# Optimization experiments

Measured on AMD Instinct MI355X. Metric: run time of the kernel, lower is better.

## Reference

```python
import jax, jax.numpy as jnp
import numpy as np

N_NODES = 100000
N_EDGES = 1600000
F_IN = 128
F_OUT = 32
HEADS = 8
ALPHA = 0.2  # LeakyReLU slope


def setup_inputs() -> dict:
    key = jax.random.key(0)
    ks = jax.random.split(key, 7)
    x = jax.random.normal(ks[0], (N_NODES, F_IN), dtype=jnp.float32)
    row = jnp.sort(jax.random.randint(ks[1], (N_EDGES,), 0, N_NODES, dtype=jnp.int32))
    col = jax.random.randint(ks[2], (N_EDGES,), 0, N_NODES, dtype=jnp.int32)
    kernels = jax.random.normal(ks[3], (HEADS, F_IN, F_OUT), dtype=jnp.float32) * 0.1
    att_self = jax.random.normal(ks[4], (HEADS, F_OUT), dtype=jnp.float32) * 0.1
    att_neigh = jax.random.normal(ks[5], (HEADS, F_OUT), dtype=jnp.float32) * 0.1
    biases = jax.random.normal(ks[6], (HEADS, F_OUT), dtype=jnp.float32) * 0.1
    return {"x": x, "row": row, "col": col, "kernels": kernels,
            "att_self": att_self, "att_neigh": att_neigh, "biases": biases}


def reference(x, row, col, kernels, att_self, att_neigh, biases):
    # GraphAttention (GAT), eval mode (dropout inactive), concat over heads.
    N = x.shape[0]
    outs = []
    for h in range(kernels.shape[0]):  # fixed small head loop
        feat = x @ kernels[h]                     # [N, F_OUT]
        a_s = feat @ att_self[h]                  # [N]
        a_n = feat @ att_neigh[h]                 # [N]
        e = a_s[row] + a_n[col]                   # [E] edge logits (SDDMM)
        e = jnp.where(e > 0, e, ALPHA * e)        # LeakyReLU(0.2)
        # row-wise (destination-node) sparse softmax, numerically stable
        m = jax.ops.segment_max(e, row, num_segments=N)
        ex = jnp.exp(e - m[row])
        denom = jax.ops.segment_sum(ex, row, num_segments=N)
        alpha = ex / denom[row]                   # [E]
        # SpMM: out[i] = sum_{e: row[e]=i} alpha[e] * feat[col[e]]
        msg = alpha[:, None] * feat[col]          # [E, F_OUT]
        out = jax.ops.segment_sum(msg, row, num_segments=N) + biases[h]
        outs.append(out)
    return jnp.concatenate(outs, axis=1)          # [N, HEADS*F_OUT]
```

## Files before the change

kernel.cpp:

```cpp
#include <hip/hip_runtime.h>
#include <hip/hip_bf16.h>
#include <math.h>


#define F_IN   128
#define F_ALL  256
#define HEADS  8
#define F_OUT  32
#define ALPHA  0.2f

using f32x4  = __attribute__((ext_vector_type(4))) float;
using bf16x8 = __attribute__((ext_vector_type(8))) short;

static __device__ __forceinline__ unsigned short f32_to_bf16(float f) {
  union { float f; unsigned u; } v; v.f = f;
  unsigned r = v.u + 0x7FFF + ((v.u >> 16) & 1);
  return (unsigned short)(r >> 16);
}
static __device__ __forceinline__ unsigned cvt_pk_bf16(float lo, float hi) {
  unsigned r;
  asm("v_cvt_pk_bf16_f32 %0, %1, %2" : "=v"(r) : "v"(lo), "v"(hi));
  return r;
}
static __device__ __forceinline__ float bf16_lo(unsigned d) {
  return __uint_as_float(d << 16);
}
static __device__ __forceinline__ float bf16_hi(unsigned d) {
  return __uint_as_float(d & 0xffff0000u);
}

__global__ __launch_bounds__(256) void prep0(const float* __restrict__ kern,
                                             const float* __restrict__ att_s,
                                             const float* __restrict__ att_n,
                                             const int* __restrict__ row,
                                             unsigned short* __restrict__ Wt,
                                             float* __restrict__ ws,
                                             float* __restrict__ wn,
                                             int* __restrict__ ptr,
                                             int N, int E) {
  int id = blockIdx.x * 256 + threadIdx.x;
  if (id < 2 * HEADS * F_IN) {
    int which = id >> 10;
    int hk = id & 1023;
    int h = hk >> 7, k = hk & 127;
    const float* att = which ? att_n : att_s;
    float s = 0.f;
#pragma unroll
    for (int f = 0; f < F_OUT; ++f)
      s += kern[(size_t)h * (F_IN * F_OUT) + k * F_OUT + f] * att[h * F_OUT + f];
    (which ? wn : ws)[hk] = s;
  } else if (id < 4096) {
    int base = (id - 2048) * 16;
#pragma unroll
    for (int i = base; i < base + 16; ++i) {
      int c = i >> 7, k = i & 127;
      Wt[i] = f32_to_bf16(kern[(size_t)(c >> 5) * (F_IN * F_OUT) + k * F_OUT + (c & 31)]);
    }
  }
  if (id <= N) {
    int lo = 0, hi = E;
    while (lo < hi) {
      int mid = (lo + hi) >> 1;
      if (row[mid] < id) lo = mid + 1; else hi = mid;
    }
    ptr[id] = lo;
  }
}

__global__ __launch_bounds__(256) void aproj_conv(const float* __restrict__ x,
                                                  const float* __restrict__ ws,
                                                  const float* __restrict__ wn,
                                                  unsigned short* __restrict__ xb,
                                                  float* __restrict__ a_s,
                                                  float* __restrict__ a_n, int N) {
  const int t = threadIdx.x;
  const int l = t & 63;
  const int o = l & 15, q = l >> 4;
  const int wid = (blockIdx.x * 256 + t) >> 6;
  const int nw  = (gridDim.x * 256) >> 6;

  const float* wrow = (o < 8 ? ws + o * F_IN : wn + (o - 8) * F_IN) + q * 32;
  float4 wv[8];
#pragma unroll
  for (int i = 0; i < 8; i++) wv[i] = reinterpret_cast<const float4*>(wrow)[i];

  for (int n = wid; n < N; n += nw) {
    const float4* xr = reinterpret_cast<const float4*>(x + (size_t)n * F_IN + q * 32);
    float acc = 0.f;
#pragma unroll
    for (int i = 0; i < 8; i++) {
      float4 xv = xr[i];
      acc += xv.x * wv[i].x + xv.y * wv[i].y + xv.z * wv[i].z + xv.w * wv[i].w;
    }
    acc += __shfl_xor(acc, 16);
    acc += __shfl_xor(acc, 32);
    if (l < 16) {
      if (o < 8) a_s[n * HEADS + o] = acc;
      else       a_n[n * HEADS + (o - 8)] = acc;
    }
    if (q == 0) {
      const float4* xc = reinterpret_cast<const float4*>(x + (size_t)n * F_IN + o * 8);
      float4 y0 = xc[0], y1 = xc[1];
      uint4 pk;
      pk.x = cvt_pk_bf16(y0.x, y0.y);
      pk.y = cvt_pk_bf16(y0.z, y0.w);
      pk.z = cvt_pk_bf16(y1.x, y1.y);
      pk.w = cvt_pk_bf16(y1.z, y1.w);
      *reinterpret_cast<uint4*>(xb + (size_t)n * F_IN + o * 8) = pk;
    }
  }
}

__global__ __launch_bounds__(256) void feat_gemm_mfma(
    const unsigned short* __restrict__ xb,
    const unsigned short* __restrict__ Wt,
    unsigned short* __restrict__ featb,
    int N) {
  const int t  = threadIdx.x;
  const int w  = t >> 6;
  const int l  = t & 63;
  const int lr = l & 15;
  const int lq = l >> 4;
  const int n0 = blockIdx.x * 64 + w * 16;

  f32x4 acc[16];
#pragma unroll
  for (int ct = 0; ct < 16; ++ct) acc[ct] = (f32x4){0.f, 0.f, 0.f, 0.f};

  int ar = n0 + lr; if (ar >= N) ar = N - 1;
  const unsigned short* xrow = xb + (size_t)ar * F_IN + lq * 8;
  bf16x8 xfr[4];
#pragma unroll
  for (int kc = 0; kc < 4; ++kc)
    xfr[kc] = *reinterpret_cast<const bf16x8*>(xrow + kc * 32);

#pragma unroll
  for (int ct = 0; ct < 16; ++ct) {
    const unsigned short* wrow = Wt + (size_t)(ct * 16 + lr) * F_IN + lq * 8;
#pragma unroll
    for (int kc = 0; kc < 4; ++kc) {
      bf16x8 wfr = *reinterpret_cast<const bf16x8*>(wrow + kc * 32);
      acc[ct] = __builtin_amdgcn_mfma_f32_16x16x32_bf16(wfr, xfr[kc], acc[ct], 0, 0, 0);
    }
  }
  if (n0 + lr < N) {
    unsigned short* frow = featb + (size_t)ar * F_ALL + lq * 4;
#pragma unroll
    for (int ct = 0; ct < 16; ++ct) {
      uint2 v;
      v.x = cvt_pk_bf16(acc[ct][0], acc[ct][1]);
      v.y = cvt_pk_bf16(acc[ct][2], acc[ct][3]);
      *reinterpret_cast<uint2*>(frow + ct * 16) = v;
    }
  }
}

__global__ __launch_bounds__(256) void gat_scatter(
    const unsigned short* __restrict__ featb,
    const float* __restrict__ a_s, const float* __restrict__ a_n,
    const int* __restrict__ col, const int* __restrict__ ptr,
    const float* __restrict__ biases, float* __restrict__ out, int N) {
  const int t  = threadIdx.x;
  const int n  = blockIdx.x * 4 + (t >> 6);
  if (n >= N) return;
  const int l  = t & 63;
  const int j  = l >> 4;
  const int q  = l & 15;
  const int h0 = 2 * j + (q >> 3);
  const int obase = j * 64 + q * 4;
  const size_t dbase = (size_t)j * 32 + q * 2;

  const int start = ptr[n];
  const int deg   = ptr[n + 1] - start;

  const float4 bv = *reinterpret_cast<const float4*>(&biases[obase]);
  if (deg == 0) {
    *reinterpret_cast<float4*>(&out[(size_t)n * F_ALL + obase]) = bv;
    return;
  }

  const float as = a_s[n * HEADS + h0];
  const unsigned* fu32 = reinterpret_cast<const unsigned*>(featb);

  float a0 = 0.f, a1 = 0.f, a2 = 0.f, a3 = 0.f, sm = 0.f;

  if (deg <= 32) {
    const int le = l & 31;
    int creg = (le < deg) ? col[start + le] : 0;
#pragma unroll 4
    for (int e = 0; e < deg; ++e) {
      int c = __shfl(creg, e, 32);
      float an = a_n[c * HEADS + h0];
      float v = as + an;
      v = v > 0.f ? v : ALPHA * v;
      float w = __expf(v);
      sm += w;
      uint2 d = *reinterpret_cast<const uint2*>(fu32 + (size_t)c * 128 + dbase);
      a0 = fmaf(w, bf16_lo(d.x), a0);
      a1 = fmaf(w, bf16_hi(d.x), a1);
      a2 = fmaf(w, bf16_lo(d.y), a2);
      a3 = fmaf(w, bf16_hi(d.y), a3);
    }
  } else {
    for (int e = 0; e < deg; ++e) {
      int c = col[start + e];
      float an = a_n[c * HEADS + h0];
      float v = as + an;
      v = v > 0.f ? v : ALPHA * v;
      float w = __expf(v);
      sm += w;
      uint2 d = *reinterpret_cast<const uint2*>(fu32 + (size_t)c * 128 + dbase);
      a0 = fmaf(w, bf16_lo(d.x), a0);
      a1 = fmaf(w, bf16_hi(d.x), a1);
      a2 = fmaf(w, bf16_lo(d.y), a2);
      a3 = fmaf(w, bf16_hi(d.y), a3);
    }
  }

  const float inv = 1.0f / sm;
  float4 o = {a0 * inv + bv.x, a1 * inv + bv.y, a2 * inv + bv.z, a3 * inv + bv.w};
  *reinterpret_cast<float4*>(&out[(size_t)n * F_ALL + obase]) = o;
}

extern "C" void kernel_launch(void* const* d_in, const int* in_sizes, int n_in,
                              void* d_out, int out_size, void* d_ws, size_t ws_size,
                              hipStream_t stream) {
  const float* x      = (const float*)d_in[0];
  const int*   row    = (const int*)d_in[1];
  const int*   col    = (const int*)d_in[2];
  const float* kern   = (const float*)d_in[3];
  const float* att_s  = (const float*)d_in[4];
  const float* att_n  = (const float*)d_in[5];
  const float* biases = (const float*)d_in[6];

  const int N = in_sizes[0] / F_IN;
  const int E = in_sizes[1];

  unsigned short* featb = (unsigned short*)d_ws;
  unsigned short* xb    = featb + (size_t)N * F_ALL;
  unsigned short* Wt    = xb + (size_t)N * F_IN;
  float* ws  = (float*)(Wt + F_ALL * F_IN);
  float* wn  = ws + HEADS * F_IN;
  float* a_s = wn + HEADS * F_IN;
  float* a_n = a_s + (size_t)N * HEADS;
  int*   ptr = (int*)(a_n + (size_t)N * HEADS);
  float* out = (float*)d_out;

  hipLaunchKernelGGL(prep0, dim3((N + 1 + 255) / 256), dim3(256), 0, stream,
                     kern, att_s, att_n, row, Wt, ws, wn, ptr, N, E);
  hipLaunchKernelGGL(aproj_conv, dim3(2048), dim3(256), 0, stream,
                     x, ws, wn, xb, a_s, a_n, N);
  hipLaunchKernelGGL(feat_gemm_mfma, dim3((N + 63) / 64), dim3(256), 0, stream,
                     xb, Wt, featb, N);
  hipLaunchKernelGGL(gat_scatter, dim3((N + 3) / 4), dim3(256), 0, stream,
                     featb, a_s, a_n, col, ptr, biases, out, N);
}
```

Baseline: 271.6 us.

## Compute edge attention weights once per edge-head and share via shuffles

Lane mapping changes to head = lane&7 and a feature chunk of lane>>3. Each lane now computes the exp weight for a single (edge, head) pair, and these weights are broadcast through wave shuffles. Before, every lane recomputed the a_n gather and exp for every edge. The separate paths for short and long rows are merged into one loop over chunks of 32 edges, and the softmax denominator is reduced across lanes at the end. This adds shuffle traffic and changes the feature-load pattern, so coalescing within a wave differs.

```diff
diff --git a/kernel.cpp b/kernel.cpp
--- a/kernel.cpp
+++ b/kernel.cpp
@@ -164,11 +164,10 @@
   const int n  = blockIdx.x * 4 + (t >> 6);
   if (n >= N) return;
   const int l  = t & 63;
-  const int j  = l >> 4;
-  const int q  = l & 15;
-  const int h0 = 2 * j + (q >> 3);
-  const int obase = j * 64 + q * 4;
-  const size_t dbase = (size_t)j * 32 + q * 2;
+  const int h  = l & 7;
+  const int dp = l >> 3;
+  const int obase = h * F_OUT + dp * 4;
+  const size_t dbase = (size_t)h * 16 + dp * 2;
 
   const int start = ptr[n];
   const int deg   = ptr[n + 1] - start;
@@ -179,45 +178,46 @@
     return;
   }
 
-  const float as = a_s[n * HEADS + h0];
+  const float as = a_s[n * HEADS + h];
   const unsigned* fu32 = reinterpret_cast<const unsigned*>(featb);
 
-  float a0 = 0.f, a1 = 0.f, a2 = 0.f, a3 = 0.f, sm = 0.f;
-
-  if (deg <= 32) {
+  float a0 = 0.f, a1 = 0.f, a2 = 0.f, a3 = 0.f, smp = 0.f;
+
+  for (int cs = 0; cs < deg; cs += 32) {
     const int le = l & 31;
-    int creg = (le < deg) ? col[start + le] : 0;
-#pragma unroll 4
-    for (int e = 0; e < deg; ++e) {
-      int c = __shfl(creg, e, 32);
-      float an = a_n[c * HEADS + h0];
-      float v = as + an;
-      v = v > 0.f ? v : ALPHA * v;
-      float w = __expf(v);
-      sm += w;
-      uint2 d = *reinterpret_cast<const uint2*>(fu32 + (size_t)c * 128 + dbase);
-      a0 = fmaf(w, bf16_lo(d.x), a0);
-      a1 = fmaf(w, bf16_hi(d.x), a1);
-      a2 = fmaf(w, bf16_lo(d.y), a2);
-      a3 = fmaf(w, bf16_hi(d.y), a3);
-    }
-  } else {
-    for (int e = 0; e < deg; ++e) {
-      int c = col[start + e];
-      float an = a_n[c * HEADS + h0];
-      float v = as + an;
-      v = v > 0.f ? v : ALPHA * v;
-      float w = __expf(v);
-      sm += w;
-      uint2 d = *reinterpret_cast<const uint2*>(fu32 + (size_t)c * 128 + dbase);
-      a0 = fmaf(w, bf16_lo(d.x), a0);
-      a1 = fmaf(w, bf16_hi(d.x), a1);
-      a2 = fmaf(w, bf16_lo(d.y), a2);
-      a3 = fmaf(w, bf16_hi(d.y), a3);
-    }
-  }
-
-  const float inv = 1.0f / sm;
+    int creg = (cs + le < deg) ? col[start + cs + le] : 0;
+    const int wlim = deg - cs;
+#pragma unroll
+    for (int g = 0; g < 4; ++g) {
+      int ew = 8 * g + dp;
+      int ce = __shfl(creg, ew, 32);
+      float w = 0.f;
+      if (ew < wlim) {
+        float v = as + a_n[ce * HEADS + h];
+        v = v > 0.f ? v : ALPHA * v;
+        w = __expf(v);
+      }
+      smp += w;
+#pragma unroll
+      for (int i = 0; i < 8; ++i) {
+        int e = 8 * g + i;
+        if (e >= wlim) break;
+        float wi = __shfl(w, 8 * i + h, 64);
+        int   ci = __shfl(creg, e, 32);
+        uint2 d  = *reinterpret_cast<const uint2*>(fu32 + (size_t)ci * 128 + dbase);
+        a0 = fmaf(wi, bf16_lo(d.x), a0);
+        a1 = fmaf(wi, bf16_hi(d.x), a1);
+        a2 = fmaf(wi, bf16_lo(d.y), a2);
+        a3 = fmaf(wi, bf16_hi(d.y), a3);
+      }
+      if (8 * g + 8 >= wlim) break;
+    }
+  }
+
+  smp += __shfl_xor(smp, 8);
+  smp += __shfl_xor(smp, 16);
+  smp += __shfl_xor(smp, 32);
+  const float inv = 1.0f / smp;
   float4 o = {a0 * inv + bv.x, a1 * inv + bv.y, a2 * inv + bv.z, a3 * inv + bv.w};
   *reinterpret_cast<float4*>(&out[(size_t)n * F_ALL + obase]) = o;
 }
```

Result: slower. 309.2 us (+13.8%).

## Move x bf16 conversion into prep and run GEMM alongside attention projection

Applied to the files above, without the earlier changes.

The x-to-bf16 conversion moves into the prep kernel, which now covers every element of x with one thread per 8 values. The attention projection and the MFMA feature GEMM are merged into one launch, with the grid split by block index into GEMM blocks and projection blocks so both run concurrently. This cuts one kernel launch and lets the fp32 projection overlap the GEMM. In exchange, prep does more work and x is read twice, once in prep and once in the projection path.

```diff
diff --git a/kernel.cpp b/kernel.cpp
--- a/kernel.cpp
+++ b/kernel.cpp
@@ -11,6 +11,7 @@
 
 using f32x4  = __attribute__((ext_vector_type(4))) float;
 using bf16x8 = __attribute__((ext_vector_type(8))) short;
+using u16x8  = __attribute__((ext_vector_type(8))) unsigned short;
 
 static __device__ __forceinline__ unsigned short f32_to_bf16(float f) {
   union { float f; unsigned u; } v; v.f = f;
@@ -29,16 +30,32 @@
   return __uint_as_float(d & 0xffff0000u);
 }
 
-__global__ __launch_bounds__(256) void prep0(const float* __restrict__ kern,
-                                             const float* __restrict__ att_s,
-                                             const float* __restrict__ att_n,
-                                             const int* __restrict__ row,
-                                             unsigned short* __restrict__ Wt,
-                                             float* __restrict__ ws,
-                                             float* __restrict__ wn,
-                                             int* __restrict__ ptr,
-                                             int N, int E) {
+__global__ __launch_bounds__(256) void prep(const float* __restrict__ x,
+                                            const float* __restrict__ kern,
+                                            const float* __restrict__ att_s,
+                                            const float* __restrict__ att_n,
+                                            const int* __restrict__ row,
+                                            unsigned short* __restrict__ xb,
+                                            unsigned short* __restrict__ Wt,
+                                            float* __restrict__ ws,
+                                            float* __restrict__ wn,
+                                            int* __restrict__ ptr,
+                                            int total_x8, int N, int E) {
   int id = blockIdx.x * 256 + threadIdx.x;
+  if (id < total_x8) {
+    const float4* x4 = reinterpret_cast<const float4*>(x);
+    float4 v0 = x4[(size_t)id * 2], v1 = x4[(size_t)id * 2 + 1];
+    u16x8 o;
+    o[0] = f32_to_bf16(v0.x); o[1] = f32_to_bf16(v0.y);
+    o[2] = f32_to_bf16(v0.z); o[3] = f32_to_bf16(v0.w);
+    o[4] = f32_to_bf16(v1.x); o[5] = f32_to_bf16(v1.y);
+    o[6] = f32_to_bf16(v1.z); o[7] = f32_to_bf16(v1.w);
+    *reinterpret_cast<u16x8*>(xb + (size_t)id * 8) = o;
+  }
+  if (id < F_ALL * F_IN) {
+    int c = id >> 7, k = id & 127;
+    Wt[id] = f32_to_bf16(kern[(size_t)(c >> 5) * (F_IN * F_OUT) + k * F_OUT + (c & 31)]);
+  }
   if (id < 2 * HEADS * F_IN) {
     int which = id >> 10;
     int hk = id & 1023;
@@ -49,13 +66,6 @@
     for (int f = 0; f < F_OUT; ++f)
       s += kern[(size_t)h * (F_IN * F_OUT) + k * F_OUT + f] * att[h * F_OUT + f];
     (which ? wn : ws)[hk] = s;
-  } else if (id < 4096) {
-    int base = (id - 2048) * 16;
-#pragma unroll
-    for (int i = base; i < base + 16; ++i) {
-      int c = i >> 7, k = i & 127;
-      Wt[i] = f32_to_bf16(kern[(size_t)(c >> 5) * (F_IN * F_OUT) + k * F_OUT + (c & 31)]);
-    }
   }
   if (id <= N) {
     int lo = 0, hi = E;
@@ -67,24 +77,66 @@
   }
 }
 
-__global__ __launch_bounds__(256) void aproj_conv(const float* __restrict__ x,
-                                                  const float* __restrict__ ws,
-                                                  const float* __restrict__ wn,
-                                                  unsigned short* __restrict__ xb,
-                                                  float* __restrict__ a_s,
-                                                  float* __restrict__ a_n, int N) {
+__global__ __launch_bounds__(256) void gemm_aproj(
+    const unsigned short* __restrict__ xb,
+    const unsigned short* __restrict__ Wt,
+    const float* __restrict__ x,
+    const float* __restrict__ ws, const float* __restrict__ wn,
+    unsigned short* __restrict__ featb,
+    float* __restrict__ a_s, float* __restrict__ a_n,
+    int N, int gemm_blocks, int aproj_waves) {
   const int t = threadIdx.x;
+
+  if ((int)blockIdx.x < gemm_blocks) {
+    const int w  = t >> 6;
+    const int l  = t & 63;
+    const int lr = l & 15;
+    const int lq = l >> 4;
+    const int n0 = blockIdx.x * 64 + w * 16;
+
+    f32x4 acc[16];
+#pragma unroll
+    for (int ct = 0; ct < 16; ++ct) acc[ct] = (f32x4){0.f, 0.f, 0.f, 0.f};
+
+    int ar = n0 + lr; if (ar >= N) ar = N - 1;
+    const unsigned short* xrow = xb + (size_t)ar * F_IN + lq * 8;
+    bf16x8 xfr[4];
+#pragma unroll
+    for (int kc = 0; kc < 4; ++kc)
+      xfr[kc] = *reinterpret_cast<const bf16x8*>(xrow + kc * 32);
+
+#pragma unroll
+    for (int ct = 0; ct < 16; ++ct) {
+      const unsigned short* wrow = Wt + (size_t)(ct * 16 + lr) * F_IN + lq * 8;
+#pragma unroll
+      for (int kc = 0; kc < 4; ++kc) {
+        bf16x8 wfr = *reinterpret_cast<const bf16x8*>(wrow + kc * 32);
+        acc[ct] = __builtin_amdgcn_mfma_f32_16x16x32_bf16(wfr, xfr[kc], acc[ct], 0, 0, 0);
+      }
+    }
+    if (n0 + lr < N) {
+      unsigned short* frow = featb + (size_t)ar * F_ALL + lq * 4;
+#pragma unroll
+      for (int ct = 0; ct < 16; ++ct) {
+        uint2 v;
+        v.x = cvt_pk_bf16(acc[ct][0], acc[ct][1]);
+        v.y = cvt_pk_bf16(acc[ct][2], acc[ct][3]);
+        *reinterpret_cast<uint2*>(frow + ct * 16) = v;
+      }
+    }
+    return;
+  }
+
   const int l = t & 63;
   const int o = l & 15, q = l >> 4;
-  const int wid = (blockIdx.x * 256 + t) >> 6;
-  const int nw  = (gridDim.x * 256) >> 6;
+  const int wid = (((int)blockIdx.x - gemm_blocks) * 256 + t) >> 6;
 
   const float* wrow = (o < 8 ? ws + o * F_IN : wn + (o - 8) * F_IN) + q * 32;
   float4 wv[8];
 #pragma unroll
   for (int i = 0; i < 8; i++) wv[i] = reinterpret_cast<const float4*>(wrow)[i];
 
-  for (int n = wid; n < N; n += nw) {
+  for (int n = wid; n < N; n += aproj_waves) {
     const float4* xr = reinterpret_cast<const float4*>(x + (size_t)n * F_IN + q * 32);
     float acc = 0.f;
 #pragma unroll
@@ -97,60 +149,6 @@
     if (l < 16) {
       if (o < 8) a_s[n * HEADS + o] = acc;
       else       a_n[n * HEADS + (o - 8)] = acc;
-    }
-    if (q == 0) {
-      const float4* xc = reinterpret_cast<const float4*>(x + (size_t)n * F_IN + o * 8);
-      float4 y0 = xc[0], y1 = xc[1];
-      uint4 pk;
-      pk.x = cvt_pk_bf16(y0.x, y0.y);
-      pk.y = cvt_pk_bf16(y0.z, y0.w);
-      pk.z = cvt_pk_bf16(y1.x, y1.y);
-      pk.w = cvt_pk_bf16(y1.z, y1.w);
-      *reinterpret_cast<uint4*>(xb + (size_t)n * F_IN + o * 8) = pk;
-    }
-  }
-}
-
-__global__ __launch_bounds__(256) void feat_gemm_mfma(
-    const unsigned short* __restrict__ xb,
-    const unsigned short* __restrict__ Wt,
-    unsigned short* __restrict__ featb,
-    int N) {
-  const int t  = threadIdx.x;
-  const int w  = t >> 6;
-  const int l  = t & 63;
-  const int lr = l & 15;
-  const int lq = l >> 4;
-  const int n0 = blockIdx.x * 64 + w * 16;
-
-  f32x4 acc[16];
-#pragma unroll
-  for (int ct = 0; ct < 16; ++ct) acc[ct] = (f32x4){0.f, 0.f, 0.f, 0.f};
-
-  int ar = n0 + lr; if (ar >= N) ar = N - 1;
-  const unsigned short* xrow = xb + (size_t)ar * F_IN + lq * 8;
-  bf16x8 xfr[4];
-#pragma unroll
-  for (int kc = 0; kc < 4; ++kc)
-    xfr[kc] = *reinterpret_cast<const bf16x8*>(xrow + kc * 32);
-
-#pragma unroll
-  for (int ct = 0; ct < 16; ++ct) {
-    const unsigned short* wrow = Wt + (size_t)(ct * 16 + lr) * F_IN + lq * 8;
-#pragma unroll
-    for (int kc = 0; kc < 4; ++kc) {
-      bf16x8 wfr = *reinterpret_cast<const bf16x8*>(wrow + kc * 32);
-      acc[ct] = __builtin_amdgcn_mfma_f32_16x16x32_bf16(wfr, xfr[kc], acc[ct], 0, 0, 0);
-    }
-  }
-  if (n0 + lr < N) {
-    unsigned short* frow = featb + (size_t)ar * F_ALL + lq * 4;
-#pragma unroll
-    for (int ct = 0; ct < 16; ++ct) {
-      uint2 v;
-      v.x = cvt_pk_bf16(acc[ct][0], acc[ct][1]);
-      v.y = cvt_pk_bf16(acc[ct][2], acc[ct][3]);
-      *reinterpret_cast<uint2*>(frow + ct * 16) = v;
     }
   }
 }
@@ -246,12 +244,15 @@
   int*   ptr = (int*)(a_n + (size_t)N * HEADS);
   float* out = (float*)d_out;
 
-  hipLaunchKernelGGL(prep0, dim3((N + 1 + 255) / 256), dim3(256), 0, stream,
-                     kern, att_s, att_n, row, Wt, ws, wn, ptr, N, E);
-  hipLaunchKernelGGL(aproj_conv, dim3(2048), dim3(256), 0, stream,
-                     x, ws, wn, xb, a_s, a_n, N);
-  hipLaunchKernelGGL(feat_gemm_mfma, dim3((N + 63) / 64), dim3(256), 0, stream,
-                     xb, Wt, featb, N);
+  const int total_x8     = N * F_IN / 8;
+  const int gemm_blocks  = (N + 63) / 64;
+  const int aproj_blocks = 1024;
+  const int aproj_waves  = aproj_blocks * 4;
+
+  hipLaunchKernelGGL(prep, dim3((total_x8 + 255) / 256), dim3(256), 0, stream,
+                     x, kern, att_s, att_n, row, xb, Wt, ws, wn, ptr, total_x8, N, E);
+  hipLaunchKernelGGL(gemm_aproj, dim3(gemm_blocks + aproj_blocks), dim3(256), 0, stream,
+                     xb, Wt, x, ws, wn, featb, a_s, a_n, N, gemm_blocks, aproj_waves);
   hipLaunchKernelGGL(gat_scatter, dim3((N + 3) / 4), dim3(256), 0, stream,
                      featb, a_s, a_n, col, ptr, biases, out, N);
 }
```

New measurement: 260.1 us (median of 2 runs). 1.04x faster.
